# Performance work log

Measured on AMD Instinct MI355X. Metric: run time of the kernel, lower is better.

## Reference

```python
import jax, jax.numpy as jnp
import numpy as np
import math

SR = 96000.0
FRAME = 2048
NB = 16
GAIN_RANGE = (-24.0, 24.0)
Q_RANGE = (0.5, 16.0)
BROADBAND = (-60.0, 0.0)
HPF_R = (20.0, 500.0)
LPF_R = (5000.0, 20000.0)
SHELF_R = (50.0, 16000.0)
PEAK_R = (100.0, 15000.0)


def _dfreq(n, rng):
    lo, hi = math.log(rng[0]), math.log(rng[1])
    return jnp.exp(lo + n * (hi - lo))


def _dgain(n, rng=GAIN_RANGE):
    return rng[0] + n * (rng[1] - rng[0])


def _dq(n):
    lo, hi = math.log(Q_RANGE[0]), math.log(Q_RANGE[1])
    return jnp.exp(lo + n * (hi - lo))


def _coeffs(ftype, fc, gain_db, Q):
    # returns stacked [g, k, a1, a2, a3, m0, m1, m2], each same shape as fc
    g = jnp.clip(jnp.tan(math.pi * fc / SR), 1e-6, 100.0)
    Q = jnp.clip(Q, 0.1, 100.0)
    one = jnp.ones_like(g)
    zero = jnp.zeros_like(g)
    if ftype in ('highpass', 'lowpass'):
        k = 1.0 / Q
        a1 = 1.0 / (1.0 + g * (g + k)); a2 = g * a1; a3 = g * a2
        if ftype == 'highpass':
            m0, m1, m2 = one, -k, -one
        else:
            m0, m1, m2 = zero, zero, one
    elif ftype == 'peak':
        A = jnp.power(10.0, gain_db / 40.0)
        k = jnp.where(gain_db >= 0, 1.0 / (Q * A), A / Q)
        a1 = 1.0 / (1.0 + g * (g + k)); a2 = g * a1; a3 = g * a2
        m0, m1, m2 = one, k * (A * A - 1.0), zero
    elif ftype == 'lowshelf':
        A = jnp.power(10.0, gain_db / 40.0); sA = jnp.sqrt(A); k = 1.0 / Q
        gs = jnp.where(gain_db >= 0, g / sA, g * sA)
        a1 = 1.0 / (1.0 + gs * (gs + k)); a2 = gs * a1; a3 = gs * a2
        m0, m1, m2 = one, k * (A - 1.0), A * A - 1.0
    else:  # highshelf
        A = jnp.power(10.0, gain_db / 40.0); sA = jnp.sqrt(A); k = 1.0 / Q
        gs = jnp.where(gain_db >= 0, g * sA, g / sA)
        a1 = 1.0 / (1.0 + gs * (gs + k)); a2 = gs * a1; a3 = gs * a2
        m0, m1, m2 = A * A, k * (1.0 - A) * A, 1.0 - A * A
    return jnp.stack([g, k, a1, a2, a3, m0, m1, m2], 0)


def _all_coeffs(params, n_frames_audio):
    # params: (B, 50, n_frames_params) -> coeffs (nF, NB, 8, B), in/out gains (nF, B)
    B = params.shape[0]
    nFp = params.shape[2]
    pidx = jnp.minimum(jnp.arange(n_frames_audio), nFp - 1)
    fp = jnp.take(params, pidx, axis=2)                 # (B, 50, nF)
    bq = fp[:, :NB * 3, :].reshape(B, NB, 3, n_frames_audio)
    in_g = jnp.power(10.0, _dgain(fp[:, -2, :], BROADBAND) / 20.0)   # (B, nF)
    out_g = jnp.power(10.0, _dgain(fp[:, -1, :], BROADBAND) / 20.0)  # (B, nF)
    cs = []
    for i in range(NB):
        fn, gn, qn = bq[:, i, 0], bq[:, i, 1], bq[:, i, 2]  # (B, nF)
        Q = _dq(qn)
        if i == 0:
            c = _coeffs('highpass', _dfreq(fn, HPF_R), None, Q)
        elif i == 15:
            c = _coeffs('lowpass', _dfreq(fn, LPF_R), None, Q)
        elif i == 1:
            c = _coeffs('lowshelf', _dfreq(fn, SHELF_R), _dgain(gn), Q)
        elif i == 14:
            c = _coeffs('highshelf', _dfreq(fn, SHELF_R), _dgain(gn), Q)
        else:
            c = _coeffs('peak', _dfreq(fn, PEAK_R), _dgain(gn), Q)
        cs.append(c)  # (8, B, nF)
    coeffs = jnp.transpose(jnp.stack(cs, 0), (3, 0, 1, 2))  # (nF, NB, 8, B)
    return coeffs, in_g.T, out_g.T


def _forward(audio, params):
    B, S = audio.shape
    nF = S // FRAME  # S chosen as exact multiple of FRAME
    coeffs, in_g, out_g = _all_coeffs(params, nF)
    frames = jnp.transpose(audio.reshape(B, nF, FRAME), (1, 2, 0))  # (nF, FRAME, B)

    def frame_step(states, xs):
        fr, c, ig, og = xs  # fr (FRAME,B), c (NB,8,B), ig (B,), og (B,)
        x = fr * ig[None, :]
        new_states = []
        for i in range(NB):
            a1, a2, a3 = c[i, 2], c[i, 3], c[i, 4]
            m0, m1, m2 = c[i, 5], c[i, 6], c[i, 7]

            def samp(st, xn, a1=a1, a2=a2, a3=a3, m0=m0, m1=m1, m2=m2):
                ic1, ic2 = st
                v3 = xn - ic2
                v1 = a1 * ic1 + a2 * v3
                v2 = ic2 + a2 * v1 + a3 * v3
                out = m0 * xn + m1 * v1 + m2 * v2
                return (2.0 * v1 - ic1, 2.0 * v2 - ic2), out

            (ic1, ic2), x = jax.lax.scan(samp, (states[i, 0], states[i, 1]), x)
            new_states.append(jnp.stack([ic1, ic2], 0))
        return jnp.stack(new_states, 0), x * og[None, :]

    init = jnp.zeros((NB, 2, B), audio.dtype)
    _, out = jax.lax.scan(frame_step, init, (frames, coeffs, in_g, out_g))
    return jnp.transpose(out, (2, 0, 1)).reshape(B, S)  # (B, S)


_forward_jit = jax.jit(_forward)


def setup_inputs() -> dict:
    key = jax.random.key(0)
    k1, k2 = jax.random.split(key)
    B, S, nFp = 32, 49152, 24  # 24 frames of 2048 samples
    audio = jax.random.normal(k1, (B, S), dtype=jnp.float32) * 0.1
    params = jax.random.uniform(k2, (B, 50, nFp), dtype=jnp.float32)
    return {'audio': audio, 'params': params}


def reference(audio, params):
    return _forward_jit(audio, params)
```

## Files before the change

kernel.cpp:

```cpp
#include <hip/hip_runtime.h>
#include <math.h>

#define NBATCH 32
#define S      49152
#define NF     24
#define NB     16
#define NBLK   4
#define CHUNK  16
#define NCH    768
#define NWAVE  12

__device__ __forceinline__ float clampf(float x, float lo, float hi) {
    return fminf(fmaxf(x, lo), hi);
}

#define FOREACH_S(OP) \
    OP(s00) OP(s01) OP(s02) OP(s03) OP(s04) OP(s05) OP(s06) OP(s07) \
    OP(s08) OP(s09) OP(s10) OP(s11) OP(s12) OP(s13) OP(s14) OP(s15)

#define DECL_S(x) float x;

#define STEPA(x) { \
    const float n1_ = fmaf(t00, ic1, fmaf(t01, ic2, b0 * (x))); \
    const float n2_ = fmaf(t10, ic1, fmaf(t11, ic2, b1 * (x))); \
    ic1 = n1_; ic2 = n2_; }

#define STEPC(x) { \
    const float y_  = fmaf(c0, ic1, fmaf(c1, ic2, c2 * (x))); \
    const float n1_ = fmaf(t00, ic1, fmaf(t01, ic2, b0 * (x))); \
    const float n2_ = fmaf(t10, ic1, fmaf(t11, ic2, b1 * (x))); \
    (x) = y_; ic1 = n1_; ic2 = n2_; }

__global__ __launch_bounds__(NCH, 3)
void biquad_chain_kernel(const float* __restrict__ audio,
                         const float* __restrict__ params,
                         float* __restrict__ out,
                         unsigned int* __restrict__ ws)
{
    __shared__ float sc[NB][NF][16];
    __shared__ float sT2048[NB][NF][4];
    __shared__ float sMw[NB][NWAVE][4];
    __shared__ float sPm[NB][NWAVE][4];
    __shared__ float sWm[NB][3][4];
    __shared__ float sgain[2][NF];
    __shared__ float sagg[2][NWAVE][2];
    __shared__ float sv[NWAVE][2];
    __shared__ unsigned int sflag[NB];

    const int t       = threadIdx.x;
    const int xcd     = blockIdx.x & 7;
    const int slot_   = blockIdx.x >> 3;
    const int bt      = xcd * 4 + (slot_ & 3);
    const int quarter = slot_ >> 2;
    const int lane    = t & 63;
    const int wave    = t >> 6;
    const int frame   = quarter * 6 + (wave >> 1);

    if (t < NB * NF) {
        const int f  = t / NF;
        const int fr = t % NF;
        const float* P = params + (size_t)bt * 50 * NF;
        const float fn = P[(3 * f + 0) * NF + fr];
        const float gn = P[(3 * f + 1) * NF + fr];
        const float qn = P[(3 * f + 2) * NF + fr];

        float Q = __expf(-0.69314718f + qn * 3.4657359f);
        Q = clampf(Q, 0.1f, 100.0f);

        float lo, hi;
        int type;
        if      (f == 0)  { lo = 20.0f;   hi = 500.0f;   type = 0; }
        else if (f == 15) { lo = 5000.0f; hi = 20000.0f; type = 1; }
        else if (f == 1)  { lo = 50.0f;   hi = 16000.0f; type = 3; }
        else if (f == 14) { lo = 50.0f;   hi = 16000.0f; type = 4; }
        else              { lo = 100.0f;  hi = 15000.0f; type = 2; }

        const float fc = __expf(__logf(lo) + fn * (__logf(hi) - __logf(lo)));
        float g_ = __tanf((float)M_PI * fc / 96000.0f);
        g_ = clampf(g_, 1e-6f, 100.0f);
        const float gdb = -24.0f + 48.0f * gn;

        float a1, a2, a3, m0, m1, m2;
        if (type == 0 || type == 1) {
            const float k = 1.0f / Q;
            a1 = 1.0f / (1.0f + g_ * (g_ + k)); a2 = g_ * a1; a3 = g_ * a2;
            if (type == 0) { m0 = 1.0f; m1 = -k;   m2 = -1.0f; }
            else           { m0 = 0.0f; m1 = 0.0f; m2 = 1.0f;  }
        } else if (type == 2) {
            const float A = __expf(gdb * (2.30258509f / 40.0f));
            const float k = (gdb >= 0.0f) ? 1.0f / (Q * A) : A / Q;
            a1 = 1.0f / (1.0f + g_ * (g_ + k)); a2 = g_ * a1; a3 = g_ * a2;
            m0 = 1.0f; m1 = k * (A * A - 1.0f); m2 = 0.0f;
        } else {
            const float A  = __expf(gdb * (2.30258509f / 40.0f));
            const float sA = sqrtf(A);
            const float k  = 1.0f / Q;
            float gs;
            if (type == 3) gs = (gdb >= 0.0f) ? g_ / sA : g_ * sA;
            else           gs = (gdb >= 0.0f) ? g_ * sA : g_ / sA;
            a1 = 1.0f / (1.0f + gs * (gs + k)); a2 = gs * a1; a3 = gs * a2;
            if (type == 3) { m0 = 1.0f;  m1 = k * (A - 1.0f);      m2 = A * A - 1.0f; }
            else           { m0 = A * A; m1 = k * (1.0f - A) * A;  m2 = 1.0f - A * A; }
        }

        const float q2  = a2 * a2 + a3;
        const float t00 = 2.0f * a1 - 1.0f;
        const float t01 = -2.0f * a2;
        const float t10 = 2.0f * a1 * a2;
        const float t11 = 1.0f - 2.0f * q2;
        const float b0  = 2.0f * a2;
        const float b1  = 2.0f * q2;
        const float c0  = a1 * (m1 + m2 * a2);
        const float c1  = m2 * (1.0f - q2) - m1 * a2;
        const float c2  = m0 + m1 * a2 + m2 * q2;

        float u00 = t00, u01 = t01, u10 = t10, u11 = t11;
        #pragma unroll
        for (int i = 0; i < 4; i++) {
            const float n00 = u00 * u00 + u01 * u10;
            const float n01 = u00 * u01 + u01 * u11;
            const float n10 = u10 * u00 + u11 * u10;
            const float n11 = u10 * u01 + u11 * u11;
            u00 = n00; u01 = n01; u10 = n10; u11 = n11;
        }
        sc[f][fr][0] = t00; sc[f][fr][1] = t01; sc[f][fr][2] = t10; sc[f][fr][3] = t11;
        sc[f][fr][4] = b0;  sc[f][fr][5] = b1;  sc[f][fr][6] = c0;  sc[f][fr][7] = c1;
        sc[f][fr][8] = c2;  sc[f][fr][9] = u00; sc[f][fr][10] = u01; sc[f][fr][11] = u10;
        sc[f][fr][12] = u11;

        #pragma unroll
        for (int i = 0; i < 6; i++) {
            const float n00 = u00 * u00 + u01 * u10;
            const float n01 = u00 * u01 + u01 * u11;
            const float n10 = u10 * u00 + u11 * u10;
            const float n11 = u10 * u01 + u11 * u11;
            u00 = n00; u01 = n01; u10 = n10; u11 = n11;
        }
        const int lf = fr - quarter * 6;
        if (lf >= 0 && lf < 6) {
            sMw[f][2 * lf][0] = u00; sMw[f][2 * lf][1] = u01;
            sMw[f][2 * lf][2] = u10; sMw[f][2 * lf][3] = u11;
            sMw[f][2 * lf + 1][0] = u00; sMw[f][2 * lf + 1][1] = u01;
            sMw[f][2 * lf + 1][2] = u10; sMw[f][2 * lf + 1][3] = u11;
        }
        {
            const float n00 = u00 * u00 + u01 * u10;
            const float n01 = u00 * u01 + u01 * u11;
            const float n10 = u10 * u00 + u11 * u10;
            const float n11 = u10 * u01 + u11 * u11;
            sT2048[f][fr][0] = n00; sT2048[f][fr][1] = n01;
            sT2048[f][fr][2] = n10; sT2048[f][fr][3] = n11;
        }
    }
    if (t >= 384 && t < 384 + 2 * NF) {
        const int idx = t - 384;
        const int which = idx / NF;
        const int fr    = idx % NF;
        const float* P = params + (size_t)bt * 50 * NF;
        const float p  = P[(48 + which) * NF + fr];
        const float db = -60.0f + 60.0f * p;
        sgain[which][fr] = __expf(db * (2.30258509f / 20.0f));
    }
    if (t < NB) sflag[t] = 0u;
    __syncthreads();

    if (t < NB) {
        const int f = t;
        float q00 = 1.0f, q01 = 0.0f, q10 = 0.0f, q11 = 1.0f;
        #pragma unroll
        for (int k = 0; k < 6; k++) {
            sPm[f][2 * k][0] = q00; sPm[f][2 * k][1] = q01;
            sPm[f][2 * k][2] = q10; sPm[f][2 * k][3] = q11;
            const float m00 = sMw[f][2 * k][0], m01 = sMw[f][2 * k][1];
            const float m10 = sMw[f][2 * k][2], m11 = sMw[f][2 * k][3];
            sPm[f][2 * k + 1][0] = m00 * q00 + m01 * q10;
            sPm[f][2 * k + 1][1] = m00 * q01 + m01 * q11;
            sPm[f][2 * k + 1][2] = m10 * q00 + m11 * q10;
            sPm[f][2 * k + 1][3] = m10 * q01 + m11 * q11;
            const float g00 = sT2048[f][quarter * 6 + k][0], g01 = sT2048[f][quarter * 6 + k][1];
            const float g10 = sT2048[f][quarter * 6 + k][2], g11 = sT2048[f][quarter * 6 + k][3];
            const float n00 = g00 * q00 + g01 * q10;
            const float n01 = g00 * q01 + g01 * q11;
            const float n10 = g10 * q00 + g11 * q10;
            const float n11 = g10 * q01 + g11 * q11;
            q00 = n00; q01 = n01; q10 = n10; q11 = n11;
        }
        if (quarter > 0) {
            float r00 = 1.0f, r01 = 0.0f, r10 = 0.0f, r11 = 1.0f;
            for (int k = quarter - 1; k >= 0; k--) {
                sWm[f][k][0] = r00; sWm[f][k][1] = r01;
                sWm[f][k][2] = r10; sWm[f][k][3] = r11;
                if (k > 0) {
                    float b00 = 1.0f, b01 = 0.0f, b10 = 0.0f, b11 = 1.0f;
                    #pragma unroll
                    for (int m = 0; m < 6; m++) {
                        const float g00 = sT2048[f][6 * k + m][0], g01 = sT2048[f][6 * k + m][1];
                        const float g10 = sT2048[f][6 * k + m][2], g11 = sT2048[f][6 * k + m][3];
                        const float n00 = g00 * b00 + g01 * b10;
                        const float n01 = g00 * b01 + g01 * b11;
                        const float n10 = g10 * b00 + g11 * b10;
                        const float n11 = g10 * b01 + g11 * b11;
                        b00 = n00; b01 = n01; b10 = n10; b11 = n11;
                    }
                    const float n00 = r00 * b00 + r01 * b10;
                    const float n01 = r00 * b01 + r01 * b11;
                    const float n10 = r10 * b00 + r11 * b10;
                    const float n11 = r10 * b01 + r11 * b11;
                    r00 = n00; r01 = n01; r10 = n10; r11 = n11;
                }
            }
        }
    }
    __syncthreads();

    FOREACH_S(DECL_S)
    {
        const float ing = sgain[0][frame];
        const float* base = audio + (size_t)bt * S
                          + (size_t)(quarter * NCH + t) * CHUNK;
        float4 q;
        q = *(const float4*)(base +  0); s00 = q.x*ing; s01 = q.y*ing; s02 = q.z*ing; s03 = q.w*ing;
        q = *(const float4*)(base +  4); s04 = q.x*ing; s05 = q.y*ing; s06 = q.z*ing; s07 = q.w*ing;
        q = *(const float4*)(base +  8); s08 = q.x*ing; s09 = q.y*ing; s10 = q.z*ing; s11 = q.w*ing;
        q = *(const float4*)(base + 12); s12 = q.x*ing; s13 = q.y*ing; s14 = q.z*ing; s15 = q.w*ing;
    }

    #pragma unroll 1
    for (int f = 0; f < NB; f++) {
        const float4 q0 = *(const float4*)&sc[f][frame][0];
        const float4 q1 = *(const float4*)&sc[f][frame][4];
        const float4 q2 = *(const float4*)&sc[f][frame][8];
        const float  M11v = sc[f][frame][12];
        const float t00 = q0.x, t01 = q0.y, t10 = q0.z, t11 = q0.w;
        const float b0  = q1.x, b1  = q1.y, c0  = q1.z, c1  = q1.w;
        const float c2  = q2.x;

        float ic1 = 0.0f, ic2 = 0.0f;
        FOREACH_S(STEPA)

        float Md00 = q2.y, Md01 = q2.z, Md10 = q2.w, Md11 = M11v;
        float Ac0 = ic1, Ac1 = ic2;
        #pragma unroll
        for (int d = 1; d < 64; d <<= 1) {
            const float lc0 = __shfl_up(Ac0, d);
            const float lc1 = __shfl_up(Ac1, d);
            if (lane >= d) {
                Ac0 = fmaf(Md00, lc0, fmaf(Md01, lc1, Ac0));
                Ac1 = fmaf(Md10, lc0, fmaf(Md11, lc1, Ac1));
            }
            const float n00 = Md00 * Md00 + Md01 * Md10;
            const float n01 = Md00 * Md01 + Md01 * Md11;
            const float n10 = Md10 * Md00 + Md11 * Md10;
            const float n11 = Md10 * Md01 + Md11 * Md11;
            Md00 = n00; Md01 = n01; Md10 = n10; Md11 = n11;
        }

        const int buf = f & 1;
        if (lane == 63) {
            sagg[buf][wave][0] = Ac0;
            sagg[buf][wave][1] = Ac1;
        }
        __syncthreads();

        const unsigned int tag = (unsigned int)(f + 1);
        unsigned int* stagebase = ws + ((size_t)(bt * NB + f) * NBLK) * 8;

        if (wave == 0) {
            float Pc0 = 0.0f, Pc1 = 0.0f;
            #pragma unroll
            for (int j = 0; j < NWAVE; j++) {
                const float a0 = sagg[buf][j][0];
                const float a1v = sagg[buf][j][1];
                const float m00 = sMw[f][j][0], m01 = sMw[f][j][1];
                const float m10 = sMw[f][j][2], m11 = sMw[f][j][3];
                if (lane > j) {
                    const float n0 = fmaf(m00, Pc0, fmaf(m01, Pc1, a0));
                    const float n1 = fmaf(m10, Pc0, fmaf(m11, Pc1, a1v));
                    Pc0 = n0; Pc1 = n1;
                }
            }

            if (quarter < NBLK - 1 && lane == NWAVE) {
                unsigned int* slot = stagebase + quarter * 8;
                float* dp = (float*)(slot + 1);
                __hip_atomic_store(&dp[0], Pc0, __ATOMIC_RELAXED, __HIP_MEMORY_SCOPE_AGENT);
                __hip_atomic_store(&dp[1], Pc1, __ATOMIC_RELAXED, __HIP_MEMORY_SCOPE_AGENT);
                __hip_atomic_store(slot, tag, __ATOMIC_RELEASE, __HIP_MEMORY_SCOPE_AGENT);
            }

            float S0x = 0.0f, S0y = 0.0f;
            if (quarter > 0) {
                float ux = 0.0f, uy = 0.0f;
                if (lane < quarter) {
                    unsigned int* slot = stagebase + lane * 8;
                    while (__hip_atomic_load(slot, __ATOMIC_ACQUIRE, __HIP_MEMORY_SCOPE_AGENT) != tag) {
                        __builtin_amdgcn_s_sleep(1);
                    }
                    const float* dp = (const float*)(slot + 1);
                    const float cx = __hip_atomic_load(&dp[0], __ATOMIC_RELAXED, __HIP_MEMORY_SCOPE_AGENT);
                    const float cy = __hip_atomic_load(&dp[1], __ATOMIC_RELAXED, __HIP_MEMORY_SCOPE_AGENT);
                    const float w00 = sWm[f][lane][0], w01 = sWm[f][lane][1];
                    const float w10 = sWm[f][lane][2], w11 = sWm[f][lane][3];
                    ux = fmaf(w00, cx, w01 * cy);
                    uy = fmaf(w10, cx, w11 * cy);
                }
                S0x = __shfl(ux, 0);
                S0y = __shfl(uy, 0);
                if (quarter > 1) { S0x += __shfl(ux, 1); S0y += __shfl(uy, 1); }
                if (quarter > 2) { S0x += __shfl(ux, 2); S0y += __shfl(uy, 2); }
            }

            if (lane < NWAVE) {
                const float p00 = sPm[f][lane][0], p01 = sPm[f][lane][1];
                const float p10 = sPm[f][lane][2], p11 = sPm[f][lane][3];
                sv[lane][0] = fmaf(p00, S0x, fmaf(p01, S0y, Pc0));
                sv[lane][1] = fmaf(p10, S0x, fmaf(p11, S0y, Pc1));
            }
            if (lane == 0) {
                __hip_atomic_store(&sflag[f], tag, __ATOMIC_RELEASE,
                                   __HIP_MEMORY_SCOPE_WORKGROUP);
            }
        } else {
            while (__hip_atomic_load(&sflag[f], __ATOMIC_ACQUIRE,
                                     __HIP_MEMORY_SCOPE_WORKGROUP) != tag)
                __builtin_amdgcn_s_sleep(1);
        }

        const float vx = sv[wave][0];
        const float vy = sv[wave][1];

        float ce0 = __shfl_up(Ac0, 1);
        float ce1 = __shfl_up(Ac1, 1);
        if (lane == 0) { ce0 = 0.0f; ce1 = 0.0f; }

        float w0 = vx, w1 = vy;
        float p00 = q2.y, p01 = q2.z, p10 = q2.w, p11 = M11v;
        #pragma unroll
        for (int b = 0; b < 6; b++) {
            if (lane & (1 << b)) {
                const float nw0 = fmaf(p00, w0, p01 * w1);
                const float nw1 = fmaf(p10, w0, p11 * w1);
                w0 = nw0; w1 = nw1;
            }
            if (b < 5) {
                const float n00 = p00 * p00 + p01 * p10;
                const float n01 = p00 * p01 + p01 * p11;
                const float n10 = p10 * p00 + p11 * p10;
                const float n11 = p10 * p01 + p11 * p11;
                p00 = n00; p01 = n01; p10 = n10; p11 = n11;
            }
        }
        ic1 = w0 + ce0;
        ic2 = w1 + ce1;

        FOREACH_S(STEPC)
    }

    {
        const float og = sgain[1][frame];
        float* base = out + (size_t)bt * S + (size_t)(quarter * NCH + t) * CHUNK;
        float4 q;
        q.x = s00*og; q.y = s01*og; q.z = s02*og; q.w = s03*og; *(float4*)(base +  0) = q;
        q.x = s04*og; q.y = s05*og; q.z = s06*og; q.w = s07*og; *(float4*)(base +  4) = q;
        q.x = s08*og; q.y = s09*og; q.z = s10*og; q.w = s11*og; *(float4*)(base +  8) = q;
        q.x = s12*og; q.y = s13*og; q.z = s14*og; q.w = s15*og; *(float4*)(base + 12) = q;
    }
}

extern "C" void kernel_launch(void* const* d_in, const int* in_sizes, int n_in,
                              void* d_out, int out_size, void* d_ws, size_t ws_size,
                              hipStream_t stream)
{
    const float* audio  = (const float*)d_in[0];
    const float* params = (const float*)d_in[1];
    float* out = (float*)d_out;
    unsigned int* ws = (unsigned int*)d_ws;
    biquad_chain_kernel<<<NBLK * NBATCH, NCH, 0, stream>>>(audio, params, out, ws);
}
```

Measured before the change: 122.4 us.

## Fuse next-stage local scan into current stage output pass and precompute matrix powers

The zero-state local accumulation for the next biquad stage (STEPA) is now computed inside the current stage's output loop (STEPF), so each stage makes one pass over the 16 samples per thread instead of two. Matrix powers used in the wave-level scan and the prefix fix-up are precomputed once into shared memory (spow) instead of being recomputed by repeated squaring in every stage. Shared arrays are repacked as float4/float2 and trimmed to this block's six frames. The fused loop carries more live registers, which may pressure occupancy under the launch bound, and it adds extra shared-memory loads per stage.

```diff
diff --git a/kernel.cpp b/kernel.cpp
--- a/kernel.cpp
+++ b/kernel.cpp
@@ -21,15 +21,24 @@
 #define DECL_S(x) float x;
 
 #define STEPA(x) { \
-    const float n1_ = fmaf(t00, ic1, fmaf(t01, ic2, b0 * (x))); \
-    const float n2_ = fmaf(t10, ic1, fmaf(t11, ic2, b1 * (x))); \
-    ic1 = n1_; ic2 = n2_; }
+    const float n1_ = fmaf(u00, ja, fmaf(u01, jb, e0 * (x))); \
+    const float n2_ = fmaf(u10, ja, fmaf(u11, jb, e1 * (x))); \
+    ja = n1_; jb = n2_; }
 
 #define STEPC(x) { \
-    const float y_  = fmaf(c0, ic1, fmaf(c1, ic2, c2 * (x))); \
-    const float n1_ = fmaf(t00, ic1, fmaf(t01, ic2, b0 * (x))); \
-    const float n2_ = fmaf(t10, ic1, fmaf(t11, ic2, b1 * (x))); \
+    const float y_  = fmaf(c0, ic1, fmaf(c1, ic2, c2v * (x))); \
+    const float n1_ = fmaf(t00, ic1, fmaf(t01, ic2, b0v * (x))); \
+    const float n2_ = fmaf(t10, ic1, fmaf(t11, ic2, b1v * (x))); \
     (x) = y_; ic1 = n1_; ic2 = n2_; }
+
+#define STEPF(x) { \
+    const float y_  = fmaf(c0, ic1, fmaf(c1, ic2, c2v * (x))); \
+    const float n1_ = fmaf(t00, ic1, fmaf(t01, ic2, b0v * (x))); \
+    const float n2_ = fmaf(t10, ic1, fmaf(t11, ic2, b1v * (x))); \
+    (x) = y_; ic1 = n1_; ic2 = n2_; \
+    const float m1_ = fmaf(u00, ja, fmaf(u01, jb, e0 * y_)); \
+    const float m2_ = fmaf(u10, ja, fmaf(u11, jb, e1 * y_)); \
+    ja = m1_; jb = m2_; }
 
 __global__ __launch_bounds__(NCH, 3)
 void biquad_chain_kernel(const float* __restrict__ audio,
@@ -37,14 +46,15 @@
                          float* __restrict__ out,
                          unsigned int* __restrict__ ws)
 {
-    __shared__ float sc[NB][NF][16];
-    __shared__ float sT2048[NB][NF][4];
-    __shared__ float sMw[NB][NWAVE][4];
-    __shared__ float sPm[NB][NWAVE][4];
-    __shared__ float sWm[NB][3][4];
-    __shared__ float sgain[2][NF];
-    __shared__ float sagg[2][NWAVE][2];
-    __shared__ float sv[NWAVE][2];
+    __shared__ __align__(16) float sc[NB][6][12];
+    __shared__ float4 spow[NB][6][6];
+    __shared__ float4 sMw[NB][6];
+    __shared__ float4 sPm[NB][NWAVE][1];
+    __shared__ float4 sWm[NB][3];
+    __shared__ float4 sT2048[NB][NF];
+    __shared__ float  sgain[2][NF];
+    __shared__ float2 sagg[2][NWAVE];
+    __shared__ float2 sv[NWAVE];
     __shared__ unsigned int sflag[NB];
 
     const int t       = threadIdx.x;
@@ -54,7 +64,8 @@
     const int quarter = slot_ >> 2;
     const int lane    = t & 63;
     const int wave    = t >> 6;
-    const int frame   = quarter * 6 + (wave >> 1);
+    const int lf      = wave >> 1;
+    const int frame   = quarter * 6 + lf;
 
     if (t < NB * NF) {
         const int f  = t / NF;
@@ -114,6 +125,16 @@
         const float c1  = m2 * (1.0f - q2) - m1 * a2;
         const float c2  = m0 + m1 * a2 + m2 * q2;
 
+        const int lfr   = fr - quarter * 6;
+        const bool loc  = (lfr >= 0 && lfr < 6);
+
+        if (loc) {
+            float* d = sc[f][lfr];
+            d[0] = t00; d[1] = t01; d[2] = t10; d[3] = t11;
+            d[4] = b0;  d[5] = b1;  d[6] = c0;  d[7] = c1;
+            d[8] = c2;  d[9] = 0.0f; d[10] = 0.0f; d[11] = 0.0f;
+        }
+
         float u00 = t00, u01 = t01, u10 = t10, u11 = t11;
         #pragma unroll
         for (int i = 0; i < 4; i++) {
@@ -123,33 +144,22 @@
             const float n11 = u10 * u01 + u11 * u11;
             u00 = n00; u01 = n01; u10 = n10; u11 = n11;
         }
-        sc[f][fr][0] = t00; sc[f][fr][1] = t01; sc[f][fr][2] = t10; sc[f][fr][3] = t11;
-        sc[f][fr][4] = b0;  sc[f][fr][5] = b1;  sc[f][fr][6] = c0;  sc[f][fr][7] = c1;
-        sc[f][fr][8] = c2;  sc[f][fr][9] = u00; sc[f][fr][10] = u01; sc[f][fr][11] = u10;
-        sc[f][fr][12] = u11;
-
-        #pragma unroll
-        for (int i = 0; i < 6; i++) {
+        #pragma unroll
+        for (int j = 0; j < 6; j++) {
+            if (loc) spow[f][lfr][j] = make_float4(u00, u01, u10, u11);
             const float n00 = u00 * u00 + u01 * u10;
             const float n01 = u00 * u01 + u01 * u11;
             const float n10 = u10 * u00 + u11 * u10;
             const float n11 = u10 * u01 + u11 * u11;
             u00 = n00; u01 = n01; u10 = n10; u11 = n11;
         }
-        const int lf = fr - quarter * 6;
-        if (lf >= 0 && lf < 6) {
-            sMw[f][2 * lf][0] = u00; sMw[f][2 * lf][1] = u01;
-            sMw[f][2 * lf][2] = u10; sMw[f][2 * lf][3] = u11;
-            sMw[f][2 * lf + 1][0] = u00; sMw[f][2 * lf + 1][1] = u01;
-            sMw[f][2 * lf + 1][2] = u10; sMw[f][2 * lf + 1][3] = u11;
-        }
+        if (loc) sMw[f][lfr] = make_float4(u00, u01, u10, u11);
         {
             const float n00 = u00 * u00 + u01 * u10;
             const float n01 = u00 * u01 + u01 * u11;
             const float n10 = u10 * u00 + u11 * u10;
             const float n11 = u10 * u01 + u11 * u11;
-            sT2048[f][fr][0] = n00; sT2048[f][fr][1] = n01;
-            sT2048[f][fr][2] = n10; sT2048[f][fr][3] = n11;
+            sT2048[f][fr] = make_float4(n00, n01, n10, n11);
         }
     }
     if (t >= 384 && t < 384 + 2 * NF) {
@@ -169,37 +179,31 @@
         float q00 = 1.0f, q01 = 0.0f, q10 = 0.0f, q11 = 1.0f;
         #pragma unroll
         for (int k = 0; k < 6; k++) {
-            sPm[f][2 * k][0] = q00; sPm[f][2 * k][1] = q01;
-            sPm[f][2 * k][2] = q10; sPm[f][2 * k][3] = q11;
-            const float m00 = sMw[f][2 * k][0], m01 = sMw[f][2 * k][1];
-            const float m10 = sMw[f][2 * k][2], m11 = sMw[f][2 * k][3];
-            sPm[f][2 * k + 1][0] = m00 * q00 + m01 * q10;
-            sPm[f][2 * k + 1][1] = m00 * q01 + m01 * q11;
-            sPm[f][2 * k + 1][2] = m10 * q00 + m11 * q10;
-            sPm[f][2 * k + 1][3] = m10 * q01 + m11 * q11;
-            const float g00 = sT2048[f][quarter * 6 + k][0], g01 = sT2048[f][quarter * 6 + k][1];
-            const float g10 = sT2048[f][quarter * 6 + k][2], g11 = sT2048[f][quarter * 6 + k][3];
-            const float n00 = g00 * q00 + g01 * q10;
-            const float n01 = g00 * q01 + g01 * q11;
-            const float n10 = g10 * q00 + g11 * q10;
-            const float n11 = g10 * q01 + g11 * q11;
+            sPm[f][2 * k][0] = make_float4(q00, q01, q10, q11);
+            const float4 mw = sMw[f][k];
+            sPm[f][2 * k + 1][0] = make_float4(
+                mw.x * q00 + mw.y * q10, mw.x * q01 + mw.y * q11,
+                mw.z * q00 + mw.w * q10, mw.z * q01 + mw.w * q11);
+            const float4 g = sT2048[f][quarter * 6 + k];
+            const float n00 = g.x * q00 + g.y * q10;
+            const float n01 = g.x * q01 + g.y * q11;
+            const float n10 = g.z * q00 + g.w * q10;
+            const float n11 = g.z * q01 + g.w * q11;
             q00 = n00; q01 = n01; q10 = n10; q11 = n11;
         }
         if (quarter > 0) {
             float r00 = 1.0f, r01 = 0.0f, r10 = 0.0f, r11 = 1.0f;
             for (int k = quarter - 1; k >= 0; k--) {
-                sWm[f][k][0] = r00; sWm[f][k][1] = r01;
-                sWm[f][k][2] = r10; sWm[f][k][3] = r11;
+                sWm[f][k] = make_float4(r00, r01, r10, r11);
                 if (k > 0) {
                     float b00 = 1.0f, b01 = 0.0f, b10 = 0.0f, b11 = 1.0f;
                     #pragma unroll
                     for (int m = 0; m < 6; m++) {
-                        const float g00 = sT2048[f][6 * k + m][0], g01 = sT2048[f][6 * k + m][1];
-                        const float g10 = sT2048[f][6 * k + m][2], g11 = sT2048[f][6 * k + m][3];
-                        const float n00 = g00 * b00 + g01 * b10;
-                        const float n01 = g00 * b01 + g01 * b11;
-                        const float n10 = g10 * b00 + g11 * b10;
-                        const float n11 = g10 * b01 + g11 * b11;
+                        const float4 g = sT2048[f][6 * k + m];
+                        const float n00 = g.x * b00 + g.y * b10;
+                        const float n01 = g.x * b01 + g.y * b11;
+                        const float n10 = g.z * b00 + g.w * b10;
+                        const float n11 = g.z * b01 + g.w * b11;
                         b00 = n00; b01 = n01; b10 = n10; b11 = n11;
                     }
                     const float n00 = r00 * b00 + r01 * b10;
@@ -225,41 +229,34 @@
         q = *(const float4*)(base + 12); s12 = q.x*ing; s13 = q.y*ing; s14 = q.z*ing; s15 = q.w*ing;
     }
 
+    float ja = 0.0f, jb = 0.0f;
+    float u00, u01, u10, u11, e0, e1;
+    {
+        const float4 q0 = *(const float4*)&sc[0][lf][0];
+        const float2 q1 = *(const float2*)&sc[0][lf][4];
+        u00 = q0.x; u01 = q0.y; u10 = q0.z; u11 = q0.w;
+        e0 = q1.x; e1 = q1.y;
+        FOREACH_S(STEPA)
+    }
+
     #pragma unroll 1
     for (int f = 0; f < NB; f++) {
-        const float4 q0 = *(const float4*)&sc[f][frame][0];
-        const float4 q1 = *(const float4*)&sc[f][frame][4];
-        const float4 q2 = *(const float4*)&sc[f][frame][8];
-        const float  M11v = sc[f][frame][12];
-        const float t00 = q0.x, t01 = q0.y, t10 = q0.z, t11 = q0.w;
-        const float b0  = q1.x, b1  = q1.y, c0  = q1.z, c1  = q1.w;
-        const float c2  = q2.x;
-
-        float ic1 = 0.0f, ic2 = 0.0f;
-        FOREACH_S(STEPA)
-
-        float Md00 = q2.y, Md01 = q2.z, Md10 = q2.w, Md11 = M11v;
-        float Ac0 = ic1, Ac1 = ic2;
-        #pragma unroll
-        for (int d = 1; d < 64; d <<= 1) {
+        float Ac0 = ja, Ac1 = jb;
+        #pragma unroll
+        for (int j = 0; j < 6; j++) {
+            const float4 mm = spow[f][lf][j];
+            const int d = 1 << j;
             const float lc0 = __shfl_up(Ac0, d);
             const float lc1 = __shfl_up(Ac1, d);
             if (lane >= d) {
-                Ac0 = fmaf(Md00, lc0, fmaf(Md01, lc1, Ac0));
-                Ac1 = fmaf(Md10, lc0, fmaf(Md11, lc1, Ac1));
-            }
-            const float n00 = Md00 * Md00 + Md01 * Md10;
-            const float n01 = Md00 * Md01 + Md01 * Md11;
-            const float n10 = Md10 * Md00 + Md11 * Md10;
-            const float n11 = Md10 * Md01 + Md11 * Md11;
-            Md00 = n00; Md01 = n01; Md10 = n10; Md11 = n11;
+                const float n0 = fmaf(mm.x, lc0, fmaf(mm.y, lc1, Ac0));
+                const float n1 = fmaf(mm.z, lc0, fmaf(mm.w, lc1, Ac1));
+                Ac0 = n0; Ac1 = n1;
+            }
         }
 
         const int buf = f & 1;
-        if (lane == 63) {
-            sagg[buf][wave][0] = Ac0;
-            sagg[buf][wave][1] = Ac1;
-        }
+        if (lane == 63) sagg[buf][wave] = make_float2(Ac0, Ac1);
         __syncthreads();
 
         const unsigned int tag = (unsigned int)(f + 1);
@@ -269,13 +266,11 @@
             float Pc0 = 0.0f, Pc1 = 0.0f;
             #pragma unroll
             for (int j = 0; j < NWAVE; j++) {
-                const float a0 = sagg[buf][j][0];
-                const float a1v = sagg[buf][j][1];
-                const float m00 = sMw[f][j][0], m01 = sMw[f][j][1];
-                const float m10 = sMw[f][j][2], m11 = sMw[f][j][3];
+                const float2 a = sagg[buf][j];
+                const float4 mw = sMw[f][j >> 1];
                 if (lane > j) {
-                    const float n0 = fmaf(m00, Pc0, fmaf(m01, Pc1, a0));
-                    const float n1 = fmaf(m10, Pc0, fmaf(m11, Pc1, a1v));
+                    const float n0 = fmaf(mw.x, Pc0, fmaf(mw.y, Pc1, a.x));
+                    const float n1 = fmaf(mw.z, Pc0, fmaf(mw.w, Pc1, a.y));
                     Pc0 = n0; Pc1 = n1;
                 }
             }
@@ -299,10 +294,9 @@
                     const float* dp = (const float*)(slot + 1);
                     const float cx = __hip_atomic_load(&dp[0], __ATOMIC_RELAXED, __HIP_MEMORY_SCOPE_AGENT);
                     const float cy = __hip_atomic_load(&dp[1], __ATOMIC_RELAXED, __HIP_MEMORY_SCOPE_AGENT);
-                    const float w00 = sWm[f][lane][0], w01 = sWm[f][lane][1];
-                    const float w10 = sWm[f][lane][2], w11 = sWm[f][lane][3];
-                    ux = fmaf(w00, cx, w01 * cy);
-                    uy = fmaf(w10, cx, w11 * cy);
+                    const float4 w = sWm[f][lane];
+                    ux = fmaf(w.x, cx, w.y * cy);
+                    uy = fmaf(w.z, cx, w.w * cy);
                 }
                 S0x = __shfl(ux, 0);
                 S0y = __shfl(uy, 0);
@@ -311,10 +305,10 @@
             }
 
             if (lane < NWAVE) {
-                const float p00 = sPm[f][lane][0], p01 = sPm[f][lane][1];
-                const float p10 = sPm[f][lane][2], p11 = sPm[f][lane][3];
-                sv[lane][0] = fmaf(p00, S0x, fmaf(p01, S0y, Pc0));
-                sv[lane][1] = fmaf(p10, S0x, fmaf(p11, S0y, Pc1));
+                const float4 pm = sPm[f][lane][0];
+                sv[lane] = make_float2(
+                    fmaf(pm.x, S0x, fmaf(pm.y, S0y, Pc0)),
+                    fmaf(pm.z, S0x, fmaf(pm.w, S0y, Pc1)));
             }
             if (lane == 0) {
                 __hip_atomic_store(&sflag[f], tag, __ATOMIC_RELEASE,
@@ -326,34 +320,41 @@
                 __builtin_amdgcn_s_sleep(1);
         }
 
-        const float vx = sv[wave][0];
-        const float vy = sv[wave][1];
+        const float2 v = sv[wave];
 
         float ce0 = __shfl_up(Ac0, 1);
         float ce1 = __shfl_up(Ac1, 1);
         if (lane == 0) { ce0 = 0.0f; ce1 = 0.0f; }
 
-        float w0 = vx, w1 = vy;
-        float p00 = q2.y, p01 = q2.z, p10 = q2.w, p11 = M11v;
+        float w0 = v.x, w1 = v.y;
         #pragma unroll
         for (int b = 0; b < 6; b++) {
+            const float4 pm = spow[f][lf][b];
             if (lane & (1 << b)) {
-                const float nw0 = fmaf(p00, w0, p01 * w1);
-                const float nw1 = fmaf(p10, w0, p11 * w1);
+                const float nw0 = fmaf(pm.x, w0, pm.y * w1);
+                const float nw1 = fmaf(pm.z, w0, pm.w * w1);
                 w0 = nw0; w1 = nw1;
             }
-            if (b < 5) {
-                const float n00 = p00 * p00 + p01 * p10;
-                const float n01 = p00 * p01 + p01 * p11;
-                const float n10 = p10 * p00 + p11 * p10;
-                const float n11 = p10 * p01 + p11 * p11;
-                p00 = n00; p01 = n01; p10 = n10; p11 = n11;
-            }
-        }
-        ic1 = w0 + ce0;
-        ic2 = w1 + ce1;
-
-        FOREACH_S(STEPC)
+        }
+        float ic1 = w0 + ce0;
+        float ic2 = w1 + ce1;
+
+        const float t00 = u00, t01 = u01, t10 = u10, t11 = u11;
+        const float b0v = e0, b1v = e1;
+        const float c0  = sc[f][lf][6];
+        const float c1  = sc[f][lf][7];
+        const float c2v = sc[f][lf][8];
+
+        if (f < NB - 1) {
+            const float4 qn = *(const float4*)&sc[f + 1][lf][0];
+            const float2 qb = *(const float2*)&sc[f + 1][lf][4];
+            u00 = qn.x; u01 = qn.y; u10 = qn.z; u11 = qn.w;
+            e0 = qb.x; e1 = qb.y;
+            ja = 0.0f; jb = 0.0f;
+            FOREACH_S(STEPF)
+        } else {
+            FOREACH_S(STEPC)
+        }
     }
 
     {
```

After: 130.7 us. 6.8% more time.

## Compute cross-wave carry redundantly per wave, removing wave-0 serialization and LDS flag

Applied to the files above, without the earlier changes.

Each wave now runs the short serial scan over earlier waves' aggregates itself and polls the inter-block stage slots directly. This removes the pattern where wave 0 computed all carries, wrote them to shared memory, and signalled the other waves through a spinning LDS flag. Shared matrices are repacked as float4 and duplicate sMw entries are dropped, so fewer shared loads and stores are issued. In exchange every wave repeats the same small scan and the same global atomic polling, which adds global atomic traffic.

```diff
diff --git a/kernel.cpp b/kernel.cpp
--- a/kernel.cpp
+++ b/kernel.cpp
@@ -37,15 +37,13 @@
                          float* __restrict__ out,
                          unsigned int* __restrict__ ws)
 {
-    __shared__ float sc[NB][NF][16];
-    __shared__ float sT2048[NB][NF][4];
-    __shared__ float sMw[NB][NWAVE][4];
-    __shared__ float sPm[NB][NWAVE][4];
-    __shared__ float sWm[NB][3][4];
-    __shared__ float sgain[2][NF];
-    __shared__ float sagg[2][NWAVE][2];
-    __shared__ float sv[NWAVE][2];
-    __shared__ unsigned int sflag[NB];
+    __shared__ __align__(16) float sc[NB][NF][16];
+    __shared__ float4 sMw[NB][6];
+    __shared__ float4 sPm[NB][NWAVE];
+    __shared__ float4 sWm[NB][3];
+    __shared__ float4 sT2048[NB][NF];
+    __shared__ float  sgain[2][NF];
+    __shared__ float2 sagg[2][NWAVE];
 
     const int t       = threadIdx.x;
     const int xcd     = blockIdx.x & 7;
@@ -136,20 +134,16 @@
             const float n11 = u10 * u01 + u11 * u11;
             u00 = n00; u01 = n01; u10 = n10; u11 = n11;
         }
-        const int lf = fr - quarter * 6;
-        if (lf >= 0 && lf < 6) {
-            sMw[f][2 * lf][0] = u00; sMw[f][2 * lf][1] = u01;
-            sMw[f][2 * lf][2] = u10; sMw[f][2 * lf][3] = u11;
-            sMw[f][2 * lf + 1][0] = u00; sMw[f][2 * lf + 1][1] = u01;
-            sMw[f][2 * lf + 1][2] = u10; sMw[f][2 * lf + 1][3] = u11;
+        const int lfr = fr - quarter * 6;
+        if (lfr >= 0 && lfr < 6) {
+            sMw[f][lfr] = make_float4(u00, u01, u10, u11);
         }
         {
             const float n00 = u00 * u00 + u01 * u10;
             const float n01 = u00 * u01 + u01 * u11;
             const float n10 = u10 * u00 + u11 * u10;
             const float n11 = u10 * u01 + u11 * u11;
-            sT2048[f][fr][0] = n00; sT2048[f][fr][1] = n01;
-            sT2048[f][fr][2] = n10; sT2048[f][fr][3] = n11;
+            sT2048[f][fr] = make_float4(n00, n01, n10, n11);
         }
     }
     if (t >= 384 && t < 384 + 2 * NF) {
@@ -161,7 +155,6 @@
         const float db = -60.0f + 60.0f * p;
         sgain[which][fr] = __expf(db * (2.30258509f / 20.0f));
     }
-    if (t < NB) sflag[t] = 0u;
     __syncthreads();
 
     if (t < NB) {
@@ -169,37 +162,31 @@
         float q00 = 1.0f, q01 = 0.0f, q10 = 0.0f, q11 = 1.0f;
         #pragma unroll
         for (int k = 0; k < 6; k++) {
-            sPm[f][2 * k][0] = q00; sPm[f][2 * k][1] = q01;
-            sPm[f][2 * k][2] = q10; sPm[f][2 * k][3] = q11;
-            const float m00 = sMw[f][2 * k][0], m01 = sMw[f][2 * k][1];
-            const float m10 = sMw[f][2 * k][2], m11 = sMw[f][2 * k][3];
-            sPm[f][2 * k + 1][0] = m00 * q00 + m01 * q10;
-            sPm[f][2 * k + 1][1] = m00 * q01 + m01 * q11;
-            sPm[f][2 * k + 1][2] = m10 * q00 + m11 * q10;
-            sPm[f][2 * k + 1][3] = m10 * q01 + m11 * q11;
-            const float g00 = sT2048[f][quarter * 6 + k][0], g01 = sT2048[f][quarter * 6 + k][1];
-            const float g10 = sT2048[f][quarter * 6 + k][2], g11 = sT2048[f][quarter * 6 + k][3];
-            const float n00 = g00 * q00 + g01 * q10;
-            const float n01 = g00 * q01 + g01 * q11;
-            const float n10 = g10 * q00 + g11 * q10;
-            const float n11 = g10 * q01 + g11 * q11;
+            sPm[f][2 * k] = make_float4(q00, q01, q10, q11);
+            const float4 mw = sMw[f][k];
+            sPm[f][2 * k + 1] = make_float4(
+                mw.x * q00 + mw.y * q10, mw.x * q01 + mw.y * q11,
+                mw.z * q00 + mw.w * q10, mw.z * q01 + mw.w * q11);
+            const float4 g = sT2048[f][quarter * 6 + k];
+            const float n00 = g.x * q00 + g.y * q10;
+            const float n01 = g.x * q01 + g.y * q11;
+            const float n10 = g.z * q00 + g.w * q10;
+            const float n11 = g.z * q01 + g.w * q11;
             q00 = n00; q01 = n01; q10 = n10; q11 = n11;
         }
         if (quarter > 0) {
             float r00 = 1.0f, r01 = 0.0f, r10 = 0.0f, r11 = 1.0f;
             for (int k = quarter - 1; k >= 0; k--) {
-                sWm[f][k][0] = r00; sWm[f][k][1] = r01;
-                sWm[f][k][2] = r10; sWm[f][k][3] = r11;
+                sWm[f][k] = make_float4(r00, r01, r10, r11);
                 if (k > 0) {
                     float b00 = 1.0f, b01 = 0.0f, b10 = 0.0f, b11 = 1.0f;
                     #pragma unroll
                     for (int m = 0; m < 6; m++) {
-                        const float g00 = sT2048[f][6 * k + m][0], g01 = sT2048[f][6 * k + m][1];
-                        const float g10 = sT2048[f][6 * k + m][2], g11 = sT2048[f][6 * k + m][3];
-                        const float n00 = g00 * b00 + g01 * b10;
-                        const float n01 = g00 * b01 + g01 * b11;
-                        const float n10 = g10 * b00 + g11 * b10;
-                        const float n11 = g10 * b01 + g11 * b11;
+                        const float4 g = sT2048[f][6 * k + m];
+                        const float n00 = g.x * b00 + g.y * b10;
+                        const float n01 = g.x * b01 + g.y * b11;
+                        const float n10 = g.z * b00 + g.w * b10;
+                        const float n11 = g.z * b01 + g.w * b11;
                         b00 = n00; b01 = n01; b10 = n10; b11 = n11;
                     }
                     const float n00 = r00 * b00 + r01 * b10;
@@ -256,82 +243,65 @@
         }
 
         const int buf = f & 1;
-        if (lane == 63) {
-            sagg[buf][wave][0] = Ac0;
-            sagg[buf][wave][1] = Ac1;
-        }
+        if (lane == 63) sagg[buf][wave] = make_float2(Ac0, Ac1);
+
+        float ce0 = __shfl_up(Ac0, 1);
+        float ce1 = __shfl_up(Ac1, 1);
+        if (lane == 0) { ce0 = 0.0f; ce1 = 0.0f; }
+
         __syncthreads();
 
         const unsigned int tag = (unsigned int)(f + 1);
         unsigned int* stagebase = ws + ((size_t)(bt * NB + f) * NBLK) * 8;
 
-        if (wave == 0) {
-            float Pc0 = 0.0f, Pc1 = 0.0f;
-            #pragma unroll
-            for (int j = 0; j < NWAVE; j++) {
-                const float a0 = sagg[buf][j][0];
-                const float a1v = sagg[buf][j][1];
-                const float m00 = sMw[f][j][0], m01 = sMw[f][j][1];
-                const float m10 = sMw[f][j][2], m11 = sMw[f][j][3];
-                if (lane > j) {
-                    const float n0 = fmaf(m00, Pc0, fmaf(m01, Pc1, a0));
-                    const float n1 = fmaf(m10, Pc0, fmaf(m11, Pc1, a1v));
-                    Pc0 = n0; Pc1 = n1;
-                }
-            }
-
-            if (quarter < NBLK - 1 && lane == NWAVE) {
+        float Pc0 = 0.0f, Pc1 = 0.0f;
+        #pragma unroll
+        for (int j = 0; j < NWAVE - 1; j++) {
+            if (j < wave) {
+                const float2 a = sagg[buf][j];
+                const float4 mw = sMw[f][j >> 1];
+                const float n0 = fmaf(mw.x, Pc0, fmaf(mw.y, Pc1, a.x));
+                const float n1 = fmaf(mw.z, Pc0, fmaf(mw.w, Pc1, a.y));
+                Pc0 = n0; Pc1 = n1;
+            }
+        }
+
+        if (wave == NWAVE - 1 && quarter < NBLK - 1) {
+            const float2 a = sagg[buf][NWAVE - 1];
+            const float4 mw = sMw[f][(NWAVE - 1) >> 1];
+            const float i0 = fmaf(mw.x, Pc0, fmaf(mw.y, Pc1, a.x));
+            const float i1 = fmaf(mw.z, Pc0, fmaf(mw.w, Pc1, a.y));
+            if (lane == 0) {
                 unsigned int* slot = stagebase + quarter * 8;
                 float* dp = (float*)(slot + 1);
-                __hip_atomic_store(&dp[0], Pc0, __ATOMIC_RELAXED, __HIP_MEMORY_SCOPE_AGENT);
-                __hip_atomic_store(&dp[1], Pc1, __ATOMIC_RELAXED, __HIP_MEMORY_SCOPE_AGENT);
+                __hip_atomic_store(&dp[0], i0, __ATOMIC_RELAXED, __HIP_MEMORY_SCOPE_AGENT);
+                __hip_atomic_store(&dp[1], i1, __ATOMIC_RELAXED, __HIP_MEMORY_SCOPE_AGENT);
                 __hip_atomic_store(slot, tag, __ATOMIC_RELEASE, __HIP_MEMORY_SCOPE_AGENT);
             }
-
-            float S0x = 0.0f, S0y = 0.0f;
-            if (quarter > 0) {
-                float ux = 0.0f, uy = 0.0f;
-                if (lane < quarter) {
-                    unsigned int* slot = stagebase + lane * 8;
+        }
+
+        float S0x = 0.0f, S0y = 0.0f;
+        if (quarter > 0) {
+            #pragma unroll
+            for (int k = 0; k < NBLK - 1; k++) {
+                if (k < quarter) {
+                    unsigned int* slot = stagebase + k * 8;
                     while (__hip_atomic_load(slot, __ATOMIC_ACQUIRE, __HIP_MEMORY_SCOPE_AGENT) != tag) {
                         __builtin_amdgcn_s_sleep(1);
                     }
                     const float* dp = (const float*)(slot + 1);
                     const float cx = __hip_atomic_load(&dp[0], __ATOMIC_RELAXED, __HIP_MEMORY_SCOPE_AGENT);
                     const float cy = __hip_atomic_load(&dp[1], __ATOMIC_RELAXED, __HIP_MEMORY_SCOPE_AGENT);
-                    const float w00 = sWm[f][lane][0], w01 = sWm[f][lane][1];
-                    const float w10 = sWm[f][lane][2], w11 = sWm[f][lane][3];
-                    ux = fmaf(w00, cx, w01 * cy);
-                    uy = fmaf(w10, cx, w11 * cy);
+                    const float4 w = sWm[f][k];
+                    S0x += fmaf(w.x, cx, w.y * cy);
+                    S0y += fmaf(w.z, cx, w.w * cy);
                 }
-                S0x = __shfl(ux, 0);
-                S0y = __shfl(uy, 0);
-                if (quarter > 1) { S0x += __shfl(ux, 1); S0y += __shfl(uy, 1); }
-                if (quarter > 2) { S0x += __shfl(ux, 2); S0y += __shfl(uy, 2); }
-            }
-
-            if (lane < NWAVE) {
-                const float p00 = sPm[f][lane][0], p01 = sPm[f][lane][1];
-                const float p10 = sPm[f][lane][2], p11 = sPm[f][lane][3];
-                sv[lane][0] = fmaf(p00, S0x, fmaf(p01, S0y, Pc0));
-                sv[lane][1] = fmaf(p10, S0x, fmaf(p11, S0y, Pc1));
-            }
-            if (lane == 0) {
-                __hip_atomic_store(&sflag[f], tag, __ATOMIC_RELEASE,
-                                   __HIP_MEMORY_SCOPE_WORKGROUP);
-            }
-        } else {
-            while (__hip_atomic_load(&sflag[f], __ATOMIC_ACQUIRE,
-                                     __HIP_MEMORY_SCOPE_WORKGROUP) != tag)
-                __builtin_amdgcn_s_sleep(1);
-        }
-
-        const float vx = sv[wave][0];
-        const float vy = sv[wave][1];
-
-        float ce0 = __shfl_up(Ac0, 1);
-        float ce1 = __shfl_up(Ac1, 1);
-        if (lane == 0) { ce0 = 0.0f; ce1 = 0.0f; }
+            }
+        }
+
+        const float4 pm = sPm[f][wave];
+        const float vx = fmaf(pm.x, S0x, fmaf(pm.y, S0y, Pc0));
+        const float vy = fmaf(pm.z, S0x, fmaf(pm.w, S0y, Pc1));
 
         float w0 = vx, w1 = vy;
         float p00 = q2.y, p01 = q2.z, p10 = q2.w, p11 = M11v;
@@ -350,8 +320,9 @@
                 p00 = n00; p01 = n01; p10 = n10; p11 = n11;
             }
         }
-        ic1 = w0 + ce0;
-        ic2 = w1 + ce1;
+        float ic1r = w0 + ce0;
+        float ic2r = w1 + ce1;
+        ic1 = ic1r; ic2 = ic2r;
 
         FOREACH_S(STEPC)
     }
```

After: 351.8 us. 187% more time.
